# Kernel optimization log

Hardware: AMD Instinct MI355X
Metric: run time of the kernel (lower is better)

The kernel has to match this reference:

```python
import jax, jax.numpy as jnp
import numpy as np

EMBED = 8  # attention_dim

def setup_inputs() -> dict:
    key = jax.random.key(0)
    ks = jax.random.split(key, 10)
    B, S, F = 256, 512, 64
    d = EMBED
    return {
        "state_batch": jax.random.normal(ks[0], (B, S, F), dtype=jnp.float32),
        "proj_w": jax.random.normal(ks[1], (F, d), dtype=jnp.float32) / np.sqrt(F),
        "proj_b": jnp.zeros((d,), dtype=jnp.float32),
        "rotation": jax.random.normal(ks[2], (d, d), dtype=jnp.float32),
        "entangle": jax.random.normal(ks[3], (d, d), dtype=jnp.float32),
        "w1": jax.random.normal(ks[4], (d, 32), dtype=jnp.float32) / np.sqrt(d),
        "b1": jnp.zeros((32,), dtype=jnp.float32),
        "w2": jax.random.normal(ks[5], (32, 16), dtype=jnp.float32) / np.sqrt(32),
        "b2": jnp.zeros((16,), dtype=jnp.float32),
        "w3": jax.random.normal(ks[6], (16, 1), dtype=jnp.float32) / np.sqrt(16),
        "b3": jnp.zeros((1,), dtype=jnp.float32),
    }

def reference(state_batch, proj_w, proj_b, rotation, entangle, w1, b1, w2, b2, w3, b3):
    # project: [B,S,F] @ [F,d] -> [B,S,d]
    proj = state_batch @ proj_w + proj_b
    # self-attention with trainable rotation/entangle matrices
    q = proj @ rotation            # [B,S,d]
    k = proj @ entangle            # [B,S,d]
    scores = jax.nn.softmax(jnp.einsum('bsd,btd->bst', q, k) / np.sqrt(EMBED), axis=-1)
    attn_out = jnp.einsum('bst,btd->bsd', scores, proj)  # value = proj
    # 3-layer MLP head: d -> 32 -> 16 -> 1, squeeze last dim
    h = jax.nn.relu(attn_out @ w1 + b1)
    h = jax.nn.relu(h @ w2 + b2)
    out = (h @ w3 + b3).squeeze(-1)  # [B,S]
    return out
```

## Files before the change

kernel.cpp:

```cpp
#include <hip/hip_runtime.h>
#include <math.h>

#define SEQ 512
#define FDIM 64
#define D 8
#define NT 512
#define NP 128
#define NQ 4
#define TQ (SEQ / NQ)

typedef float v2f __attribute__((ext_vector_type(2)));

__global__ __launch_bounds__(NT, 2) void hybrid_attn_kernel(
    const float* __restrict__ state,
    const float* __restrict__ proj_w,
    const float* __restrict__ proj_b,
    const float* __restrict__ rotation,
    const float* __restrict__ entangle,
    const float* __restrict__ w1,
    const float* __restrict__ b1,
    const float* __restrict__ w2,
    const float* __restrict__ b2,
    const float* __restrict__ w3,
    const float* __restrict__ b3,
    float* __restrict__ out)
{
    __shared__ __align__(16) float s_pv[2 * SEQ * D];
    __shared__ __align__(16) float s_q[SEQ * D];
    __shared__ __align__(16) float s_mm[16 * NP];
    __shared__ __align__(16) float s_pw[FDIM * D];
    __shared__ float s_rot[D * D];
    __shared__ float s_ent[D * D];
    __shared__ float s_pb[D];
    __shared__ float s_w1[D * 32];
    __shared__ float s_b1[32];
    __shared__ float s_w2[32 * 16];
    __shared__ float s_b2[16];
    __shared__ float s_w3[16];
    __shared__ float s_b3[1];

    float* const s_proj = s_pv;
    float* const s_k    = s_pv + SEQ * D;

    const int b   = blockIdx.x;
    const int tid = threadIdx.x;

    if (tid < FDIM * D) s_pw[tid] = proj_w[tid];
    if (tid < D * D) {
        s_rot[tid] = rotation[tid];
        s_ent[tid] = entangle[tid];
    }
    if (tid < D)       s_pb[tid] = proj_b[tid];
    if (tid < D * 32)  s_w1[tid] = w1[tid];
    if (tid < 32)      s_b1[tid] = b1[tid];
    if (tid < 32 * 16) s_w2[tid] = w2[tid];
    if (tid < 16) { s_b2[tid] = b2[tid]; s_w3[tid] = w3[tid]; }
    if (tid == 0)      s_b3[0] = b3[0];
    __syncthreads();

    {
        const int r = tid;
        float pj[D];
        #pragma unroll
        for (int j = 0; j < D; j++) pj[j] = s_pb[j];

        const float4* srp = (const float4*)(state + ((size_t)b * SEQ + r) * FDIM);
        #pragma unroll
        for (int c = 0; c < FDIM / 4; c++) {
            float4 v = srp[c];
            float vs[4] = {v.x, v.y, v.z, v.w};
            #pragma unroll
            for (int e = 0; e < 4; e++) {
                #pragma unroll
                for (int j = 0; j < D; j++) pj[j] += vs[e] * s_pw[(c * 4 + e) * D + j];
            }
        }

        const float QS = 0.35355339059327373f;
        float qv[D], kv[D];
        #pragma unroll
        for (int j = 0; j < D; j++) {
            float aq = 0.f, ak = 0.f;
            #pragma unroll
            for (int i = 0; i < D; i++) {
                aq += pj[i] * s_rot[i * D + j];
                ak += pj[i] * s_ent[i * D + j];
            }
            qv[j] = aq * QS;
            kv[j] = ak;
        }

        float4* dp = (float4*)(s_proj + r * D);
        dp[0] = make_float4(pj[0], pj[1], pj[2], pj[3]);
        dp[1] = make_float4(pj[4], pj[5], pj[6], pj[7]);
        float4* dk = (float4*)(s_k + r * D);
        dk[0] = make_float4(kv[0], kv[1], kv[2], kv[3]);
        dk[1] = make_float4(kv[4], kv[5], kv[6], kv[7]);
        float4* dq = (float4*)(s_q + r * D);
        dq[0] = make_float4(qv[0], qv[1], qv[2], qv[3]);
        dq[1] = make_float4(qv[4], qv[5], qv[6], qv[7]);
    }
    __syncthreads();

    const int p    = tid & (NP - 1);
    const int qt   = tid >> 7;
    const int toff = qt * TQ;

    v2f q[4][4];
    #pragma unroll
    for (int u = 0; u < 4; u++) {
        const float4* qp = (const float4*)(s_q + (p + NP * u) * D);
        float4 x0 = qp[0], x1 = qp[1];
        q[u][0] = (v2f){x0.x, x0.y}; q[u][1] = (v2f){x0.z, x0.w};
        q[u][2] = (v2f){x1.x, x1.y}; q[u][3] = (v2f){x1.z, x1.w};
    }

    const float* kp = s_k    + toff * D;
    const float* vp = s_proj + toff * D;

    float m[4] = {-1e30f, -1e30f, -1e30f, -1e30f};
    for (int i = 0; i < TQ / 4; i++) {
        const float4* kt = (const float4*)(kp + (4 * i) * D);
        float4 ka = kt[0], kb = kt[1];
        v2f kk0 = (v2f){ka.x, ka.y}, kk1 = (v2f){ka.z, ka.w};
        v2f kk2 = (v2f){kb.x, kb.y}, kk3 = (v2f){kb.z, kb.w};
        #pragma unroll
        for (int u = 0; u < 4; u++) {
            v2f d = q[u][0] * kk0; d = q[u][1] * kk1 + d;
            d = q[u][2] * kk2 + d; d = q[u][3] * kk3 + d;
            m[u] = fmaxf(m[u], d.x + d.y);
        }
    }
    #pragma unroll
    for (int u = 0; u < 4; u++) s_mm[(u * 4 + qt) * NP + p] = m[u];
    __syncthreads();
    float nm[4];
    #pragma unroll
    for (int u = 0; u < 4; u++) {
        float mu = s_mm[(u * 4 + 0) * NP + p];
        mu = fmaxf(mu, s_mm[(u * 4 + 1) * NP + p]);
        mu = fmaxf(mu, s_mm[(u * 4 + 2) * NP + p]);
        mu = fmaxf(mu, s_mm[(u * 4 + 3) * NP + p]);
        nm[u] = -mu;
    }

    float l[4] = {0.f, 0.f, 0.f, 0.f};
    v2f acc[4][4];
    #pragma unroll
    for (int u = 0; u < 4; u++) {
        #pragma unroll
        for (int j = 0; j < 4; j++) acc[u][j] = (v2f){0.f, 0.f};
    }

    #pragma unroll 2
    for (int t = 0; t < TQ; t++) {
        const float4* kt = (const float4*)(kp + t * D);
        float4 ka = kt[0], kb = kt[1];
        v2f kk0 = (v2f){ka.x, ka.y}, kk1 = (v2f){ka.z, ka.w};
        v2f kk2 = (v2f){kb.x, kb.y}, kk3 = (v2f){kb.z, kb.w};
        const float4* vt = (const float4*)(vp + t * D);
        float4 va = vt[0], vb = vt[1];
        v2f vv0 = (v2f){va.x, va.y}, vv1 = (v2f){va.z, va.w};
        v2f vv2 = (v2f){vb.x, vb.y}, vv3 = (v2f){vb.z, vb.w};

        float e[4];
        #pragma unroll
        for (int u = 0; u < 4; u++) {
            v2f d = (v2f){nm[u], 0.f};
            d = q[u][0] * kk0 + d; d = q[u][1] * kk1 + d;
            d = q[u][2] * kk2 + d; d = q[u][3] * kk3 + d;
            e[u] = __expf(d.x + d.y);
            l[u] += e[u];
        }
        #pragma unroll
        for (int u = 0; u < 4; u++) {
            v2f ev = (v2f){e[u], e[u]};
            acc[u][0] = ev * vv0 + acc[u][0]; acc[u][1] = ev * vv1 + acc[u][1];
            acc[u][2] = ev * vv2 + acc[u][2]; acc[u][3] = ev * vv3 + acc[u][3];
        }
    }
    __syncthreads();

    float* const s_mrg = s_pv;
    #pragma unroll
    for (int rnd = 0; rnd < 2; rnd++) {
        const int ua = 2 * rnd, ub = 2 * rnd + 1;
        if (qt > 0) {
            float* dd = s_mrg + (size_t)((qt - 1) * NP + p) * 18;
            ((float4*)dd)[0] = make_float4(acc[ua][0].x, acc[ua][0].y, acc[ua][1].x, acc[ua][1].y);
            ((float4*)dd)[1] = make_float4(acc[ua][2].x, acc[ua][2].y, acc[ua][3].x, acc[ua][3].y);
            ((float4*)dd)[2] = make_float4(acc[ub][0].x, acc[ub][0].y, acc[ub][1].x, acc[ub][1].y);
            ((float4*)dd)[3] = make_float4(acc[ub][2].x, acc[ub][2].y, acc[ub][3].x, acc[ub][3].y);
            dd[16] = l[ua];
            dd[17] = l[ub];
        }
        __syncthreads();
        if (qt == 0) {
            #pragma unroll
            for (int w = 0; w < NQ - 1; w++) {
                const float* ss = s_mrg + (size_t)(w * NP + p) * 18;
                float4 u0 = ((const float4*)ss)[0], u1 = ((const float4*)ss)[1];
                float4 u2 = ((const float4*)ss)[2], u3 = ((const float4*)ss)[3];
                acc[ua][0] += (v2f){u0.x, u0.y}; acc[ua][1] += (v2f){u0.z, u0.w};
                acc[ua][2] += (v2f){u1.x, u1.y}; acc[ua][3] += (v2f){u1.z, u1.w};
                acc[ub][0] += (v2f){u2.x, u2.y}; acc[ub][1] += (v2f){u2.z, u2.w};
                acc[ub][2] += (v2f){u3.x, u3.y}; acc[ub][3] += (v2f){u3.z, u3.w};
                l[ua] += ss[16];
                l[ub] += ss[17];
            }
        }
        __syncthreads();
    }

    float* const s_attn = s_q;
    if (qt == 0) {
        #pragma unroll
        for (int u = 0; u < 4; u++) {
            const float inv = 1.0f / l[u];
            float4* dd = (float4*)(s_attn + (p + NP * u) * D);
            dd[0] = make_float4(acc[u][0].x*inv, acc[u][0].y*inv, acc[u][1].x*inv, acc[u][1].y*inv);
            dd[1] = make_float4(acc[u][2].x*inv, acc[u][2].y*inv, acc[u][3].x*inv, acc[u][3].y*inv);
        }
    }
    __syncthreads();

    {
        const float4* ap = (const float4*)(s_attn + tid * D);
        float4 a0 = ap[0], a1 = ap[1];
        float attn[D] = {a0.x, a0.y, a0.z, a0.w, a1.x, a1.y, a1.z, a1.w};

        float h1[32];
        #pragma unroll
        for (int j = 0; j < 32; j++) {
            float a = s_b1[j];
            #pragma unroll
            for (int i = 0; i < D; i++) a += attn[i] * s_w1[i * 32 + j];
            h1[j] = fmaxf(a, 0.f);
        }
        float h2[16];
        #pragma unroll
        for (int j = 0; j < 16; j++) {
            float a = s_b2[j];
            #pragma unroll
            for (int i = 0; i < 32; i++) a += h1[i] * s_w2[i * 16 + j];
            h2[j] = fmaxf(a, 0.f);
        }
        float o = s_b3[0];
        #pragma unroll
        for (int i = 0; i < 16; i++) o += h2[i] * s_w3[i];

        out[(size_t)b * SEQ + tid] = o;
    }
}

extern "C" void kernel_launch(void* const* d_in, const int* in_sizes, int n_in,
                              void* d_out, int out_size, void* d_ws, size_t ws_size,
                              hipStream_t stream) {
    const float* state    = (const float*)d_in[0];
    const float* proj_w   = (const float*)d_in[1];
    const float* proj_b   = (const float*)d_in[2];
    const float* rotation = (const float*)d_in[3];
    const float* entangle = (const float*)d_in[4];
    const float* w1       = (const float*)d_in[5];
    const float* b1       = (const float*)d_in[6];
    const float* w2       = (const float*)d_in[7];
    const float* b2       = (const float*)d_in[8];
    const float* w3       = (const float*)d_in[9];
    const float* b3       = (const float*)d_in[10];
    float* out = (float*)d_out;

    const int B = in_sizes[0] / (SEQ * FDIM);
    hybrid_attn_kernel<<<B, NT, 0, stream>>>(
        state, proj_w, proj_b, rotation, entangle,
        w1, b1, w2, b2, w3, b3, out);
}
```

Measured before the change: 131.2 us.

## Split each batch across two blocks by query half, with 8-way key split

Each batch is now handled by two blocks, each owning 256 queries, and the keys are split into 8 chunks instead of 4. The grid doubles to 512 blocks and launch bounds request 4 blocks per CU, so more work can run in parallel across the 256 CUs. The cost is that both blocks recompute the full projection and K for all 512 rows. The merge across key chunks also becomes wider and uses more barriers.

Result: slower. 144.0 us (+9.7%).

```diff
diff --git a/kernel.cpp b/kernel.cpp
--- a/kernel.cpp
+++ b/kernel.cpp
@@ -5,13 +5,13 @@
 #define FDIM 64
 #define D 8
 #define NT 512
-#define NP 128
-#define NQ 4
-#define TQ (SEQ / NQ)
+#define NP 64
+#define NE 8
+#define TE (SEQ / NE)
 
 typedef float v2f __attribute__((ext_vector_type(2)));
 
-__global__ __launch_bounds__(NT, 2) void hybrid_attn_kernel(
+__global__ __launch_bounds__(NT, 4) void hybrid_attn_kernel(
     const float* __restrict__ state,
     const float* __restrict__ proj_w,
     const float* __restrict__ proj_b,
@@ -25,9 +25,10 @@
     const float* __restrict__ b3,
     float* __restrict__ out)
 {
-    __shared__ __align__(16) float s_pv[2 * SEQ * D];
-    __shared__ __align__(16) float s_q[SEQ * D];
-    __shared__ __align__(16) float s_mm[16 * NP];
+    __shared__ __align__(16) float s_proj[SEQ * D];
+    __shared__ __align__(16) float s_k[SEQ * D];
+    __shared__ __align__(16) float s_q[256 * D];
+    __shared__ __align__(16) float s_mm[4 * NE * NP];
     __shared__ __align__(16) float s_pw[FDIM * D];
     __shared__ float s_rot[D * D];
     __shared__ float s_ent[D * D];
@@ -39,11 +40,10 @@
     __shared__ float s_w3[16];
     __shared__ float s_b3[1];
 
-    float* const s_proj = s_pv;
-    float* const s_k    = s_pv + SEQ * D;
-
-    const int b   = blockIdx.x;
-    const int tid = threadIdx.x;
+    const int bb   = blockIdx.x;
+    const int b    = bb >> 1;
+    const int half = bb & 1;
+    const int tid  = threadIdx.x;
 
     if (tid < FDIM * D) s_pw[tid] = proj_w[tid];
     if (tid < D * D) {
@@ -96,15 +96,17 @@
         float4* dk = (float4*)(s_k + r * D);
         dk[0] = make_float4(kv[0], kv[1], kv[2], kv[3]);
         dk[1] = make_float4(kv[4], kv[5], kv[6], kv[7]);
-        float4* dq = (float4*)(s_q + r * D);
-        dq[0] = make_float4(qv[0], qv[1], qv[2], qv[3]);
-        dq[1] = make_float4(qv[4], qv[5], qv[6], qv[7]);
+        if ((r >> 8) == half) {
+            float4* dq = (float4*)(s_q + (r & 255) * D);
+            dq[0] = make_float4(qv[0], qv[1], qv[2], qv[3]);
+            dq[1] = make_float4(qv[4], qv[5], qv[6], qv[7]);
+        }
     }
     __syncthreads();
 
     const int p    = tid & (NP - 1);
-    const int qt   = tid >> 7;
-    const int toff = qt * TQ;
+    const int qt   = tid >> 6;
+    const int toff = qt * TE;
 
     v2f q[4][4];
     #pragma unroll
@@ -119,7 +121,7 @@
     const float* vp = s_proj + toff * D;
 
     float m[4] = {-1e30f, -1e30f, -1e30f, -1e30f};
-    for (int i = 0; i < TQ / 4; i++) {
+    for (int i = 0; i < TE / 4; i++) {
         const float4* kt = (const float4*)(kp + (4 * i) * D);
         float4 ka = kt[0], kb = kt[1];
         v2f kk0 = (v2f){ka.x, ka.y}, kk1 = (v2f){ka.z, ka.w};
@@ -132,15 +134,14 @@
         }
     }
     #pragma unroll
-    for (int u = 0; u < 4; u++) s_mm[(u * 4 + qt) * NP + p] = m[u];
+    for (int u = 0; u < 4; u++) s_mm[(u * NE + qt) * NP + p] = m[u];
     __syncthreads();
     float nm[4];
     #pragma unroll
     for (int u = 0; u < 4; u++) {
-        float mu = s_mm[(u * 4 + 0) * NP + p];
-        mu = fmaxf(mu, s_mm[(u * 4 + 1) * NP + p]);
-        mu = fmaxf(mu, s_mm[(u * 4 + 2) * NP + p]);
-        mu = fmaxf(mu, s_mm[(u * 4 + 3) * NP + p]);
+        float mu = s_mm[(u * NE + 0) * NP + p];
+        #pragma unroll
+        for (int w = 1; w < NE; w++) mu = fmaxf(mu, s_mm[(u * NE + w) * NP + p]);
         nm[u] = -mu;
     }
 
@@ -153,7 +154,7 @@
     }
 
     #pragma unroll 2
-    for (int t = 0; t < TQ; t++) {
+    for (int t = 0; t < TE; t++) {
         const float4* kt = (const float4*)(kp + t * D);
         float4 ka = kt[0], kb = kt[1];
         v2f kk0 = (v2f){ka.x, ka.y}, kk1 = (v2f){ka.z, ka.w};
@@ -181,32 +182,27 @@
     }
     __syncthreads();
 
-    float* const s_mrg = s_pv;
-    #pragma unroll
-    for (int rnd = 0; rnd < 2; rnd++) {
-        const int ua = 2 * rnd, ub = 2 * rnd + 1;
+    float* const mrg_acc = s_q;
+    float* const mrg_l   = s_q + (NE - 1) * NP * 8;
+    #pragma unroll
+    for (int u = 0; u < 4; u++) {
         if (qt > 0) {
-            float* dd = s_mrg + (size_t)((qt - 1) * NP + p) * 18;
-            ((float4*)dd)[0] = make_float4(acc[ua][0].x, acc[ua][0].y, acc[ua][1].x, acc[ua][1].y);
-            ((float4*)dd)[1] = make_float4(acc[ua][2].x, acc[ua][2].y, acc[ua][3].x, acc[ua][3].y);
-            ((float4*)dd)[2] = make_float4(acc[ub][0].x, acc[ub][0].y, acc[ub][1].x, acc[ub][1].y);
-            ((float4*)dd)[3] = make_float4(acc[ub][2].x, acc[ub][2].y, acc[ub][3].x, acc[ub][3].y);
-            dd[16] = l[ua];
-            dd[17] = l[ub];
+            const int slot = (qt - 1) * NP + p;
+            float4* dd = (float4*)(mrg_acc + slot * 8);
+            dd[0] = make_float4(acc[u][0].x, acc[u][0].y, acc[u][1].x, acc[u][1].y);
+            dd[1] = make_float4(acc[u][2].x, acc[u][2].y, acc[u][3].x, acc[u][3].y);
+            mrg_l[slot] = l[u];
         }
         __syncthreads();
         if (qt == 0) {
             #pragma unroll
-            for (int w = 0; w < NQ - 1; w++) {
-                const float* ss = s_mrg + (size_t)(w * NP + p) * 18;
-                float4 u0 = ((const float4*)ss)[0], u1 = ((const float4*)ss)[1];
-                float4 u2 = ((const float4*)ss)[2], u3 = ((const float4*)ss)[3];
-                acc[ua][0] += (v2f){u0.x, u0.y}; acc[ua][1] += (v2f){u0.z, u0.w};
-                acc[ua][2] += (v2f){u1.x, u1.y}; acc[ua][3] += (v2f){u1.z, u1.w};
-                acc[ub][0] += (v2f){u2.x, u2.y}; acc[ub][1] += (v2f){u2.z, u2.w};
-                acc[ub][2] += (v2f){u3.x, u3.y}; acc[ub][3] += (v2f){u3.z, u3.w};
-                l[ua] += ss[16];
-                l[ub] += ss[17];
+            for (int w = 0; w < NE - 1; w++) {
+                const int slot = w * NP + p;
+                const float4* ss = (const float4*)(mrg_acc + slot * 8);
+                float4 u0 = ss[0], u1 = ss[1];
+                acc[u][0] += (v2f){u0.x, u0.y}; acc[u][1] += (v2f){u0.z, u0.w};
+                acc[u][2] += (v2f){u1.x, u1.y}; acc[u][3] += (v2f){u1.z, u1.w};
+                l[u] += mrg_l[slot];
             }
         }
         __syncthreads();
@@ -224,7 +220,7 @@
     }
     __syncthreads();
 
-    {
+    if (tid < 256) {
         const float4* ap = (const float4*)(s_attn + tid * D);
         float4 a0 = ap[0], a1 = ap[1];
         float attn[D] = {a0.x, a0.y, a0.z, a0.w, a1.x, a1.y, a1.z, a1.w};
@@ -249,7 +245,7 @@
         #pragma unroll
         for (int i = 0; i < 16; i++) o += h2[i] * s_w3[i];
 
-        out[(size_t)b * SEQ + tid] = o;
+        out[(size_t)b * SEQ + half * 256 + tid] = o;
     }
 }
 
@@ -270,7 +266,7 @@
     float* out = (float*)d_out;
 
     const int B = in_sizes[0] / (SEQ * FDIM);
-    hybrid_attn_kernel<<<B, NT, 0, stream>>>(
+    hybrid_attn_kernel<<<B * 2, NT, 0, stream>>>(
         state, proj_w, proj_b, rotation, entangle,
         w1, b1, w2, b2, w3, b3, out);
 }
```
